# Kernel tuning notes

Measured on AMD Instinct MI355X. Metric: run time of the kernel, lower is better.

Reference implementation:

```python
import jax, jax.numpy as jnp
import numpy as np

N = 4096          # num_nodes
F = 64            # node_features
H = 128           # hidden_dim
NH = 4            # num_heads
HD = H // NH      # per-head dim = 32
L = 3             # num_layers
C = 7             # num_classes
EDGE_P = 0.004    # ~16 avg degree


def setup_inputs() -> dict:
    key = jax.random.key(0)
    ks = jax.random.split(key, 20)
    g = lambda k, shape, fan_in: jax.random.normal(k, shape, jnp.float32) / np.sqrt(fan_in)
    x = jax.random.normal(ks[0], (N, F), jnp.float32)
    adj = (jax.random.uniform(ks[1], (N, N)) < EDGE_P).astype(jnp.float32)
    return {
        "x": x,
        "adj": adj,
        "enc_W": g(ks[2], (F, H), F), "enc_b": jnp.zeros((H,), jnp.float32),
        "gcn_W": g(ks[3], (L, H, H), H), "gcn_b": jnp.zeros((L, H), jnp.float32),
        "attn_W": g(ks[4], (L, NH, H, HD), H), "attn_Wb": jnp.zeros((L, NH, HD), jnp.float32),
        "attn_a": g(ks[5], (L, NH, 2 * HD), 2 * HD), "attn_ab": jnp.zeros((L, NH), jnp.float32),
        "cls_W1": g(ks[6], (H, H // 2), H), "cls_b1": jnp.zeros((H // 2,), jnp.float32),
        "cls_W2": g(ks[7], (H // 2, C), H // 2), "cls_b2": jnp.zeros((C,), jnp.float32),
        "con_W1": g(ks[8], (H, H // 2), H), "con_b1": jnp.zeros((H // 2,), jnp.float32),
        "con_W2": g(ks[9], (H // 2, 1), H // 2), "con_b2": jnp.zeros((1,), jnp.float32),
    }


def _normalize_adj(adj):
    a = adj + jnp.eye(adj.shape[0], dtype=adj.dtype)
    dinv = jnp.sum(a, axis=1) ** -0.5
    return dinv[:, None] * a * dinv[None, :]


def _gcn(h, adj_norm, W, b):
    support = adj_norm @ h                      # [N,H]
    return jax.nn.relu(support @ W + b)         # dropout=0 (eval)


def _attention(h, edge_mask, W, Wb, a, ab):
    # h:[N,H], W:[NH,H,HD], a:[NH,2*HD]; per-pair score = Linear(concat(h_i,h_j))
    hh = jnp.einsum('nf,hfd->hnd', h, W) + Wb[:, None, :]     # [NH,N,HD]
    a_src, a_dst = a[:, :HD], a[:, HD:]
    s_src = jnp.einsum('hnd,hd->hn', hh, a_src)               # [NH,N]
    s_dst = jnp.einsum('hnd,hd->hn', hh, a_dst)               # [NH,N]
    scores = s_src[:, :, None] + s_dst[:, None, :] + ab[:, None, None]
    # original uses literal 0.0 (NOT -inf) for non-edges before softmax
    scores = jnp.where(edge_mask[None, :, :], scores, 0.0)    # [NH,N,N]
    probs = jax.nn.softmax(scores, axis=-1)
    out = jnp.einsum('hij,hjd->hid', probs, hh)               # [NH,N,HD]
    return out.transpose(1, 0, 2).reshape(h.shape[0], NH * HD)


def reference(x, adj, enc_W, enc_b, gcn_W, gcn_b, attn_W, attn_Wb, attn_a, attn_ab,
              cls_W1, cls_b1, cls_W2, cls_b2, con_W1, con_b1, con_W2, con_b2):
    h = jax.nn.relu(x @ enc_W + enc_b)          # node encoder (dropout=0)
    adj_norm = _normalize_adj(adj)
    edge_mask = adj > 0
    for i in range(L):
        h_gcn = _gcn(h, adj_norm, gcn_W[i], gcn_b[i])
        h_attn = _attention(h, edge_mask, attn_W[i], attn_Wb[i], attn_a[i], attn_ab[i])
        h = jax.nn.relu(h_gcn + h_attn)
    node_logits = jax.nn.relu(h @ cls_W1 + cls_b1) @ cls_W2 + cls_b2
    h_mean = jnp.mean(h, axis=0, keepdims=True)
    contagion = jax.nn.relu(h_mean @ con_W1 + con_b1) @ con_W2 + con_b2
    return (node_logits, h, contagion)
```

## Files before the change

kernel.cpp:

```cpp
#include <hip/hip_runtime.h>

typedef unsigned short u16;
typedef unsigned int u32;

#define N 4096
#define F 64
#define H 128
#define NH 4
#define HD 32
#define EMAX 64

__device__ float g_hA[N * H];
__device__ float g_hB[N * H];
__device__ float g_hhA[N * H];
__device__ float g_hhB[N * H];
__device__ u16   g_cols[N * EMAX];
__device__ int   g_deg[N];
__device__ float g_dinv[N];
__device__ float g_ssrcA[N * NH];
__device__ float g_ssrcB[N * NH];
__device__ float g_sdstA[N * NH];
__device__ float g_sdstB[N * NH];
__device__ float g_part[3][32][H];
__device__ float g_hpart[32][H];

__device__ __forceinline__ void agg4(int i0, int tid, const float* __restrict__ h,
                                     const float* __restrict__ hhin,
                                     const float* __restrict__ ssrc_in,
                                     const float* __restrict__ sdst_in,
                                     int l, const float* __restrict__ abv,
                                     int (&jl)[4][EMAX], float (&dv)[4][EMAX],
                                     float (&sdl)[4][EMAX * NH],
                                     float& outa0, float& outa1,
                                     float& sup0, float& sup1) {
  int c = tid & 127, rg = tid >> 7, hc = c >> 5;
  int darr[4];
#pragma unroll
  for (int r = 0; r < 4; ++r) darr[r] = g_deg[i0 + r];
#pragma unroll
  for (int r = 0; r < 4; ++r) {
    const u16* cl = g_cols + (size_t)(i0 + r) * EMAX;
    for (int e = tid; e < darr[r]; e += 256) {
      int j = cl[e];
      jl[r][e] = j;
      dv[r][e] = g_dinv[j];
    }
  }
  __syncthreads();
#pragma unroll
  for (int r = 0; r < 4; ++r)
    for (int idx = tid; idx < darr[r] * NH; idx += 256)
      sdl[r][idx] = sdst_in[jl[r][idx >> 2] * NH + (idx & 3)];
  __syncthreads();

  float sumc = 0.f;
  const float* part = &g_part[l][0][0];
#pragma unroll
  for (int s = 0; s < 32; ++s) sumc += part[s * H + c];
  float ab = abv[hc];

  float oa[2], sp[2];
#pragma unroll
  for (int rr = 0; rr < 2; ++rr) {
    int r = rg * 2 + rr;
    int i = i0 + r, dd = darr[r];
    float ssrc = ssrc_in[i * NH + hc];
    float M = -INFINITY;
    for (int e = 0; e < dd; ++e) M = fmaxf(M, sdl[r][e * NH + hc]);
    float mv = fmaxf(0.f, ssrc + ab + M);
    float em = expf(-mv);
    float base = ssrc + ab - mv;
    float aA = 0.f, aT = 0.f, aG = 0.f, S = 0.f;
    int e = 0;
    for (; e + 2 <= dd; e += 2) {
      int j0 = jl[r][e], j1 = jl[r][e + 1];
      float q0 = hhin[j0 * H + c], q1 = hhin[j1 * H + c];
      float p0 = h[j0 * H + c], p1 = h[j1 * H + c];
      float w0 = expf(base + sdl[r][e * NH + hc]);
      float w1 = expf(base + sdl[r][(e + 1) * NH + hc]);
      aA = fmaf(w0, q0, aA); aA = fmaf(w1, q1, aA);
      aT += q0 + q1;
      aG = fmaf(dv[r][e], p0, aG); aG = fmaf(dv[r][e + 1], p1, aG);
      S += w0 + w1;
    }
    for (; e < dd; ++e) {
      int j = jl[r][e];
      float w = expf(base + sdl[r][e * NH + hc]);
      float q = hhin[j * H + c];
      aA = fmaf(w, q, aA);
      aT += q;
      aG = fmaf(dv[r][e], h[j * H + c], aG);
      S += w;
    }
    float Z = S + em * (float)(N - dd);
    oa[rr] = (aA + em * (sumc - aT)) / Z;
    float di = g_dinv[i];
    sp[rr] = di * (aG + di * h[i * H + c]);
  }
  outa0 = oa[0]; outa1 = oa[1]; sup0 = sp[0]; sup1 = sp[1];
}

__device__ __forceinline__ void proj4(int i0, int tid, const float (&hrowT)[H][4],
                                      const float* __restrict__ aW,
                                      const float* __restrict__ aWb,
                                      const float* __restrict__ aa, int lp,
                                      float* __restrict__ hhout,
                                      float* __restrict__ ssrc_out,
                                      float* __restrict__ sdst_out) {
  int c = tid & 127, rg = tid >> 7, hc = c >> 5, dc = c & 31;
  float b = aWb[hc * HD + dc];
  float p0 = b, p1 = b;
  for (int f = 0; f < H; ++f) {
    float w = aW[(hc * H + f) * HD + dc];
    float2 hv = *reinterpret_cast<const float2*>(&hrowT[f][rg * 2]);
    p0 = fmaf(hv.x, w, p0);
    p1 = fmaf(hv.y, w, p1);
  }
  int r0 = i0 + rg * 2, r1 = r0 + 1;
  hhout[r0 * H + c] = p0;
  hhout[r1 * H + c] = p1;
  const float* ap = aa + hc * 2 * HD;
  float as = ap[dc], ad = ap[HD + dc];
  float ss0 = p0 * as, ss1 = p1 * as, sd0 = p0 * ad, sd1 = p1 * ad;
#pragma unroll
  for (int m = 16; m >= 1; m >>= 1) {
    ss0 += __shfl_xor(ss0, m, 64); ss1 += __shfl_xor(ss1, m, 64);
    sd0 += __shfl_xor(sd0, m, 64); sd1 += __shfl_xor(sd1, m, 64);
  }
  if (dc == 0) {
    ssrc_out[r0 * NH + hc] = ss0; ssrc_out[r1 * NH + hc] = ss1;
    sdst_out[r0 * NH + hc] = sd0; sdst_out[r1 * NH + hc] = sd1;
  }
  atomicAdd(&g_part[lp][r0 & 31][c], p0);
  atomicAdd(&g_part[lp][r1 & 31][c], p1);
}

__global__ void k_prep(const float* __restrict__ adj, const float* __restrict__ x,
                       const float* __restrict__ eW, const float* __restrict__ eb,
                       const float* __restrict__ aW, const float* __restrict__ aWb,
                       const float* __restrict__ aa) {
  __shared__ float xT[F][4];
  __shared__ float hrowT[H][4];
  __shared__ int   cnt4[4];
  int i0 = blockIdx.x * 4, tid = threadIdx.x;
  int c = tid & 127, rg = tid >> 7;

  if (tid < 4) cnt4[tid] = 0;
  __syncthreads();
  {
    int r = tid >> 6, u = tid & 63;
    int row = i0 + r;
    const float4* p = reinterpret_cast<const float4*>(adj + (size_t)row * N) + u;
#pragma unroll
    for (int k = 0; k < 16; ++k) {
      float4 v = p[k * 64];
      int base = (u + k * 64) * 4;
      if (v.x != 0.f) { int q = atomicAdd(&cnt4[r], 1); if (q < EMAX) g_cols[row * EMAX + q] = (u16)(base); }
      if (v.y != 0.f) { int q = atomicAdd(&cnt4[r], 1); if (q < EMAX) g_cols[row * EMAX + q] = (u16)(base + 1); }
      if (v.z != 0.f) { int q = atomicAdd(&cnt4[r], 1); if (q < EMAX) g_cols[row * EMAX + q] = (u16)(base + 2); }
      if (v.w != 0.f) { int q = atomicAdd(&cnt4[r], 1); if (q < EMAX) g_cols[row * EMAX + q] = (u16)(base + 3); }
    }
    xT[tid & 63][tid >> 6] = x[(i0 + (tid >> 6)) * F + (tid & 63)];
  }
  __syncthreads();
  if (tid < 4) {
    int cnt = cnt4[tid];
    g_deg[i0 + tid] = cnt < EMAX ? cnt : EMAX;
    g_dinv[i0 + tid] = 1.0f / sqrtf((float)(cnt + 1));
  }

  float b = eb[c];
  float e0 = b, e1 = b;
  for (int k = 0; k < F; ++k) {
    float w = eW[k * H + c];
    float2 xv = *reinterpret_cast<const float2*>(&xT[k][rg * 2]);
    e0 = fmaf(xv.x, w, e0);
    e1 = fmaf(xv.y, w, e1);
  }
  e0 = fmaxf(e0, 0.f); e1 = fmaxf(e1, 0.f);
  int r0 = i0 + rg * 2, r1 = r0 + 1;
  g_hA[r0 * H + c] = e0; g_hA[r1 * H + c] = e1;
  hrowT[c][rg * 2] = e0; hrowT[c][rg * 2 + 1] = e1;
  __syncthreads();
  proj4(i0, tid, hrowT, aW, aWb, aa, 0, g_hhA, g_ssrcA, g_sdstA);
}

__global__ void k_acp(int pp, int l, const float* __restrict__ gW,
                      const float* __restrict__ gb, const float* __restrict__ aW,
                      const float* __restrict__ aWb, const float* __restrict__ aa,
                      const float* __restrict__ abv) {
  const float* h    = pp ? g_hB : g_hA;
  float*       hout = pp ? g_hA : g_hB;
  const float* hhin = pp ? g_hhB : g_hhA;
  float*       hhout= pp ? g_hhA : g_hhB;
  const float* ssin = pp ? g_ssrcB : g_ssrcA;
  float*       ssout= pp ? g_ssrcA : g_ssrcB;
  const float* sdin = pp ? g_sdstB : g_sdstA;
  float*       sdout= pp ? g_sdstA : g_sdstB;
  __shared__ int   jl[4][EMAX];
  __shared__ float dv[4][EMAX];
  __shared__ float sdl[4][EMAX * NH];
  __shared__ float srowT[H][4];
  __shared__ float hrowT[H][4];
  int i0 = blockIdx.x * 4, tid = threadIdx.x;
  int c = tid & 127, rg = tid >> 7;

  float oa0, oa1, sp0, sp1;
  agg4(i0, tid, h, hhin, ssin, sdin, l, abv, jl, dv, sdl, oa0, oa1, sp0, sp1);
  srowT[c][rg * 2] = sp0; srowT[c][rg * 2 + 1] = sp1;
  __syncthreads();

  float b = gb[c];
  float a0 = b, a1 = b;
  for (int f = 0; f < H; ++f) {
    float w = gW[f * H + c];
    float2 sv = *reinterpret_cast<const float2*>(&srowT[f][rg * 2]);
    a0 = fmaf(sv.x, w, a0);
    a1 = fmaf(sv.y, w, a1);
  }
  float g0 = fmaxf(fmaxf(a0, 0.f) + oa0, 0.f);
  float g1 = fmaxf(fmaxf(a1, 0.f) + oa1, 0.f);
  int r0 = i0 + rg * 2, r1 = r0 + 1;
  hout[r0 * H + c] = g0; hout[r1 * H + c] = g1;
  hrowT[c][rg * 2] = g0; hrowT[c][rg * 2 + 1] = g1;
  __syncthreads();

  proj4(i0, tid, hrowT, aW, aWb, aa, l + 1, hhout, ssout, sdout);
}

__global__ void k_acc(const float* __restrict__ abv, const float* __restrict__ gW,
                      const float* __restrict__ gb,
                      const float* __restrict__ W1, const float* __restrict__ b1,
                      const float* __restrict__ W2, const float* __restrict__ b2,
                      float* __restrict__ out, float* __restrict__ outh) {
  __shared__ int   jl[4][EMAX];
  __shared__ float dv[4][EMAX];
  __shared__ float sdl[4][EMAX * NH];
  __shared__ float srowT[H][4];
  __shared__ float hrowT[H][4];
  __shared__ float tl[4][64];
  int i0 = blockIdx.x * 4, tid = threadIdx.x;
  int c = tid & 127, rg = tid >> 7;

  float oa0, oa1, sp0, sp1;
  agg4(i0, tid, g_hA, g_hhA, g_ssrcA, g_sdstA, 2, abv, jl, dv, sdl, oa0, oa1, sp0, sp1);
  srowT[c][rg * 2] = sp0; srowT[c][rg * 2 + 1] = sp1;
  __syncthreads();

  float b = gb[c];
  float a0 = b, a1 = b;
  for (int f = 0; f < H; ++f) {
    float w = gW[f * H + c];
    float2 sv = *reinterpret_cast<const float2*>(&srowT[f][rg * 2]);
    a0 = fmaf(sv.x, w, a0);
    a1 = fmaf(sv.y, w, a1);
  }
  float g0 = fmaxf(fmaxf(a0, 0.f) + oa0, 0.f);
  float g1 = fmaxf(fmaxf(a1, 0.f) + oa1, 0.f);
  int r0 = i0 + rg * 2, r1 = r0 + 1;
  outh[r0 * H + c] = g0; outh[r1 * H + c] = g1;
  hrowT[c][rg * 2] = g0; hrowT[c][rg * 2 + 1] = g1;
  atomicAdd(&g_hpart[r0 & 31][c], g0);
  atomicAdd(&g_hpart[r1 & 31][c], g1);
  __syncthreads();

  int u = tid & 63, rr4 = tid >> 6;
  float a2 = b1[u];
  for (int f = 0; f < H; ++f) a2 = fmaf(hrowT[f][rr4], W1[f * 64 + u], a2);
  tl[rr4][u] = fmaxf(a2, 0.f);
  __syncthreads();
  if (tid < 28) {
    int r = tid / 7, j = tid - r * 7;
    float p = b2[j];
    for (int v = 0; v < 64; ++v) p = fmaf(tl[r][v], W2[v * 7 + j], p);
    out[(i0 + r) * 7 + j] = p;
  }
}

__global__ void k_contagion(const float* __restrict__ W1, const float* __restrict__ b1,
                            const float* __restrict__ W2, const float* __restrict__ b2,
                            float* __restrict__ out) {
  __shared__ float hm[H];
  __shared__ float tl[64];
  int tid = threadIdx.x;
  {
    float s = 0.f;
#pragma unroll
    for (int sl = 0; sl < 32; ++sl) s += g_hpart[sl][tid];
    hm[tid] = s * (1.0f / 4096.0f);
  }
  __syncthreads();
  if (tid < 64) {
    float acc = b1[tid];
    for (int f = 0; f < H; ++f) acc = fmaf(hm[f], W1[f * 64 + tid], acc);
    tl[tid] = fmaxf(acc, 0.f);
  }
  __syncthreads();
  if (tid == 0) {
    float p = b2[0];
    for (int v = 0; v < 64; ++v) p = fmaf(tl[v], W2[v], p);
    out[0] = p;
  }
  float* pz = &g_part[0][0][0];
  for (int i = tid; i < 3 * 32 * H; i += 128) pz[i] = 0.f;
  float* hz = &g_hpart[0][0];
  for (int i = tid; i < 32 * H; i += 128) hz[i] = 0.f;
}

extern "C" void kernel_launch(void* const* d_in, const int* in_sizes, int n_in,
                              void* d_out, int out_size, void* d_ws, size_t ws_size,
                              hipStream_t stream) {
  const float* x       = (const float*)d_in[0];
  const float* adj     = (const float*)d_in[1];
  const float* enc_W   = (const float*)d_in[2];
  const float* enc_b   = (const float*)d_in[3];
  const float* gcn_W   = (const float*)d_in[4];
  const float* gcn_b   = (const float*)d_in[5];
  const float* attn_W  = (const float*)d_in[6];
  const float* attn_Wb = (const float*)d_in[7];
  const float* attn_a  = (const float*)d_in[8];
  const float* attn_ab = (const float*)d_in[9];
  const float* cls_W1  = (const float*)d_in[10];
  const float* cls_b1  = (const float*)d_in[11];
  const float* cls_W2  = (const float*)d_in[12];
  const float* cls_b2  = (const float*)d_in[13];
  const float* con_W1  = (const float*)d_in[14];
  const float* con_b1  = (const float*)d_in[15];
  const float* con_W2  = (const float*)d_in[16];
  const float* con_b2  = (const float*)d_in[17];
  (void)in_sizes; (void)n_in; (void)d_ws; (void)ws_size; (void)out_size;

  float* out = (float*)d_out;
  float* outh = out + (size_t)N * 7;
  float* outc = out + (size_t)N * 7 + (size_t)N * H;

  k_prep<<<N / 4, 256, 0, stream>>>(adj, x, enc_W, enc_b, attn_W, attn_Wb, attn_a);
  k_acp<<<N / 4, 256, 0, stream>>>(0, 0, gcn_W, gcn_b,
                                   attn_W + (size_t)1 * NH * H * HD,
                                   attn_Wb + (size_t)1 * NH * HD,
                                   attn_a + (size_t)1 * NH * 2 * HD, attn_ab);
  k_acp<<<N / 4, 256, 0, stream>>>(1, 1, gcn_W + (size_t)1 * H * H, gcn_b + H,
                                   attn_W + (size_t)2 * NH * H * HD,
                                   attn_Wb + (size_t)2 * NH * HD,
                                   attn_a + (size_t)2 * NH * 2 * HD, attn_ab + NH);
  k_acc<<<N / 4, 256, 0, stream>>>(attn_ab + 2 * NH, gcn_W + (size_t)2 * H * H,
                                   gcn_b + 2 * H, cls_W1, cls_b1, cls_W2, cls_b2,
                                   out, outh);
  k_contagion<<<1, 128, 0, stream>>>(con_W1, con_b1, con_W2, con_b2, outc);
}
```

Baseline: 232.6 us.

## Process eight rows per block with two columns per thread and float2 loads

Each block now handles 8 nodes instead of 4, and each thread owns two adjacent feature columns, using float2 loads and stores for gathers, weights and outputs. Each weight load now feeds four FMAs instead of two, which cuts weight-read traffic per node and halves the block count. Shared arrays are padded to width 10. The price is more registers per thread and fewer blocks (512) to spread across CUs, which may lower latency hiding in the gather-heavy aggregation.

```diff
diff --git a/kernel.cpp b/kernel.cpp
--- a/kernel.cpp
+++ b/kernel.cpp
@@ -9,6 +9,8 @@
 #define NH 4
 #define HD 32
 #define EMAX 64
+#define BR 8
+#define PAD 10
 
 __device__ float g_hA[N * H];
 __device__ float g_hB[N * H];
@@ -24,23 +26,66 @@
 __device__ float g_part[3][32][H];
 __device__ float g_hpart[32][H];
 
-__device__ __forceinline__ void agg4(int i0, int tid, const float* __restrict__ h,
+__device__ __forceinline__ void proj8(int i0, int tid, const float (&hrowT)[H][PAD],
+                                      const float* __restrict__ aW,
+                                      const float* __restrict__ aWb,
+                                      const float* __restrict__ aa, int lp,
+                                      float* __restrict__ hhout,
+                                      float* __restrict__ ssrc_out,
+                                      float* __restrict__ sdst_out) {
+  int c2 = tid & 63, rg = tid >> 6;
+  int c0 = c2 * 2, hc = c0 >> 5, dc = c0 & 31;
+  float2 bb = *reinterpret_cast<const float2*>(&aWb[hc * HD + dc]);
+  float p00 = bb.x, p01 = bb.y, p10 = bb.x, p11 = bb.y;
+  for (int f = 0; f < H; ++f) {
+    float2 w = *reinterpret_cast<const float2*>(&aW[(hc * H + f) * HD + dc]);
+    float2 hv = *reinterpret_cast<const float2*>(&hrowT[f][rg * 2]);
+    p00 = fmaf(hv.x, w.x, p00); p01 = fmaf(hv.x, w.y, p01);
+    p10 = fmaf(hv.y, w.x, p10); p11 = fmaf(hv.y, w.y, p11);
+  }
+  int r0 = i0 + rg * 2, r1 = r0 + 1;
+  *reinterpret_cast<float2*>(&hhout[r0 * H + c0]) = make_float2(p00, p01);
+  *reinterpret_cast<float2*>(&hhout[r1 * H + c0]) = make_float2(p10, p11);
+  const float* ap = aa + hc * 2 * HD;
+  float2 as = *reinterpret_cast<const float2*>(&ap[dc]);
+  float2 ad = *reinterpret_cast<const float2*>(&ap[HD + dc]);
+  float ss0 = p00 * as.x + p01 * as.y;
+  float ss1 = p10 * as.x + p11 * as.y;
+  float sd0 = p00 * ad.x + p01 * ad.y;
+  float sd1 = p10 * ad.x + p11 * ad.y;
+#pragma unroll
+  for (int m = 8; m >= 1; m >>= 1) {
+    ss0 += __shfl_xor(ss0, m, 64); ss1 += __shfl_xor(ss1, m, 64);
+    sd0 += __shfl_xor(sd0, m, 64); sd1 += __shfl_xor(sd1, m, 64);
+  }
+  if ((c2 & 15) == 0) {
+    ssrc_out[r0 * NH + hc] = ss0; ssrc_out[r1 * NH + hc] = ss1;
+    sdst_out[r0 * NH + hc] = sd0; sdst_out[r1 * NH + hc] = sd1;
+  }
+  atomicAdd(&g_part[lp][r0 & 31][c0], p00);
+  atomicAdd(&g_part[lp][r0 & 31][c0 + 1], p01);
+  atomicAdd(&g_part[lp][r1 & 31][c0], p10);
+  atomicAdd(&g_part[lp][r1 & 31][c0 + 1], p11);
+}
+
+__device__ __forceinline__ void agg8(int i0, int tid, const float* __restrict__ h,
                                      const float* __restrict__ hhin,
                                      const float* __restrict__ ssrc_in,
                                      const float* __restrict__ sdst_in,
                                      int l, const float* __restrict__ abv,
-                                     int (&jl)[4][EMAX], float (&dv)[4][EMAX],
-                                     float (&sdl)[4][EMAX * NH],
-                                     float& outa0, float& outa1,
-                                     float& sup0, float& sup1) {
-  int c = tid & 127, rg = tid >> 7, hc = c >> 5;
-  int darr[4];
-#pragma unroll
-  for (int r = 0; r < 4; ++r) darr[r] = g_deg[i0 + r];
-#pragma unroll
-  for (int r = 0; r < 4; ++r) {
+                                     int (&jl)[BR][EMAX], float (&dv)[BR][EMAX],
+                                     float (&sdl)[BR][EMAX * NH],
+                                     float2& outa0, float2& outa1,
+                                     float2& sup0, float2& sup1) {
+  int c2 = tid & 63, rg = tid >> 6;
+  int c0 = c2 * 2, hc = c0 >> 5;
+  int dloc[BR];
+#pragma unroll
+  for (int r = 0; r < BR; ++r) dloc[r] = g_deg[i0 + r];
+#pragma unroll
+  for (int r = 0; r < BR; ++r) {
     const u16* cl = g_cols + (size_t)(i0 + r) * EMAX;
-    for (int e = tid; e < darr[r]; e += 256) {
+    for (int e = tid; e < dloc[r]; e += 256) {
       int j = cl[e];
       jl[r][e] = j;
       dv[r][e] = g_dinv[j];
@@ -48,141 +93,122 @@
   }
   __syncthreads();
 #pragma unroll
-  for (int r = 0; r < 4; ++r)
-    for (int idx = tid; idx < darr[r] * NH; idx += 256)
+  for (int r = 0; r < BR; ++r)
+    for (int idx = tid; idx < dloc[r] * NH; idx += 256)
       sdl[r][idx] = sdst_in[jl[r][idx >> 2] * NH + (idx & 3)];
   __syncthreads();
 
-  float sumc = 0.f;
+  float sumc0 = 0.f, sumc1 = 0.f;
   const float* part = &g_part[l][0][0];
 #pragma unroll
-  for (int s = 0; s < 32; ++s) sumc += part[s * H + c];
+  for (int s = 0; s < 32; ++s) {
+    sumc0 += part[s * H + c0];
+    sumc1 += part[s * H + c0 + 1];
+  }
   float ab = abv[hc];
 
-  float oa[2], sp[2];
+  float2 oa[2], sp[2];
 #pragma unroll
   for (int rr = 0; rr < 2; ++rr) {
     int r = rg * 2 + rr;
-    int i = i0 + r, dd = darr[r];
+    int i = i0 + r, dd = dloc[r];
     float ssrc = ssrc_in[i * NH + hc];
     float M = -INFINITY;
     for (int e = 0; e < dd; ++e) M = fmaxf(M, sdl[r][e * NH + hc]);
     float mv = fmaxf(0.f, ssrc + ab + M);
     float em = expf(-mv);
     float base = ssrc + ab - mv;
-    float aA = 0.f, aT = 0.f, aG = 0.f, S = 0.f;
+    float aA0 = 0.f, aA1 = 0.f, aT0 = 0.f, aT1 = 0.f, aG0 = 0.f, aG1 = 0.f, S = 0.f;
     int e = 0;
     for (; e + 2 <= dd; e += 2) {
       int j0 = jl[r][e], j1 = jl[r][e + 1];
-      float q0 = hhin[j0 * H + c], q1 = hhin[j1 * H + c];
-      float p0 = h[j0 * H + c], p1 = h[j1 * H + c];
+      float2 q0 = *reinterpret_cast<const float2*>(&hhin[j0 * H + c0]);
+      float2 q1 = *reinterpret_cast<const float2*>(&hhin[j1 * H + c0]);
+      float2 p0 = *reinterpret_cast<const float2*>(&h[j0 * H + c0]);
+      float2 p1 = *reinterpret_cast<const float2*>(&h[j1 * H + c0]);
       float w0 = expf(base + sdl[r][e * NH + hc]);
       float w1 = expf(base + sdl[r][(e + 1) * NH + hc]);
-      aA = fmaf(w0, q0, aA); aA = fmaf(w1, q1, aA);
-      aT += q0 + q1;
-      aG = fmaf(dv[r][e], p0, aG); aG = fmaf(dv[r][e + 1], p1, aG);
+      aA0 = fmaf(w0, q0.x, aA0); aA0 = fmaf(w1, q1.x, aA0);
+      aA1 = fmaf(w0, q0.y, aA1); aA1 = fmaf(w1, q1.y, aA1);
+      aT0 += q0.x + q1.x; aT1 += q0.y + q1.y;
+      aG0 = fmaf(dv[r][e], p0.x, aG0); aG0 = fmaf(dv[r][e + 1], p1.x, aG0);
+      aG1 = fmaf(dv[r][e], p0.y, aG1); aG1 = fmaf(dv[r][e + 1], p1.y, aG1);
       S += w0 + w1;
     }
     for (; e < dd; ++e) {
       int j = jl[r][e];
+      float2 q = *reinterpret_cast<const float2*>(&hhin[j * H + c0]);
+      float2 p = *reinterpret_cast<const float2*>(&h[j * H + c0]);
       float w = expf(base + sdl[r][e * NH + hc]);
-      float q = hhin[j * H + c];
-      aA = fmaf(w, q, aA);
-      aT += q;
-      aG = fmaf(dv[r][e], h[j * H + c], aG);
+      aA0 = fmaf(w, q.x, aA0); aA1 = fmaf(w, q.y, aA1);
+      aT0 += q.x; aT1 += q.y;
+      aG0 = fmaf(dv[r][e], p.x, aG0); aG1 = fmaf(dv[r][e], p.y, aG1);
       S += w;
     }
     float Z = S + em * (float)(N - dd);
-    oa[rr] = (aA + em * (sumc - aT)) / Z;
+    oa[rr] = make_float2((aA0 + em * (sumc0 - aT0)) / Z,
+                         (aA1 + em * (sumc1 - aT1)) / Z);
     float di = g_dinv[i];
-    sp[rr] = di * (aG + di * h[i * H + c]);
+    float2 hvi = *reinterpret_cast<const float2*>(&h[i * H + c0]);
+    sp[rr] = make_float2(di * (aG0 + di * hvi.x), di * (aG1 + di * hvi.y));
   }
   outa0 = oa[0]; outa1 = oa[1]; sup0 = sp[0]; sup1 = sp[1];
-}
-
-__device__ __forceinline__ void proj4(int i0, int tid, const float (&hrowT)[H][4],
-                                      const float* __restrict__ aW,
-                                      const float* __restrict__ aWb,
-                                      const float* __restrict__ aa, int lp,
-                                      float* __restrict__ hhout,
-                                      float* __restrict__ ssrc_out,
-                                      float* __restrict__ sdst_out) {
-  int c = tid & 127, rg = tid >> 7, hc = c >> 5, dc = c & 31;
-  float b = aWb[hc * HD + dc];
-  float p0 = b, p1 = b;
-  for (int f = 0; f < H; ++f) {
-    float w = aW[(hc * H + f) * HD + dc];
-    float2 hv = *reinterpret_cast<const float2*>(&hrowT[f][rg * 2]);
-    p0 = fmaf(hv.x, w, p0);
-    p1 = fmaf(hv.y, w, p1);
-  }
-  int r0 = i0 + rg * 2, r1 = r0 + 1;
-  hhout[r0 * H + c] = p0;
-  hhout[r1 * H + c] = p1;
-  const float* ap = aa + hc * 2 * HD;
-  float as = ap[dc], ad = ap[HD + dc];
-  float ss0 = p0 * as, ss1 = p1 * as, sd0 = p0 * ad, sd1 = p1 * ad;
-#pragma unroll
-  for (int m = 16; m >= 1; m >>= 1) {
-    ss0 += __shfl_xor(ss0, m, 64); ss1 += __shfl_xor(ss1, m, 64);
-    sd0 += __shfl_xor(sd0, m, 64); sd1 += __shfl_xor(sd1, m, 64);
-  }
-  if (dc == 0) {
-    ssrc_out[r0 * NH + hc] = ss0; ssrc_out[r1 * NH + hc] = ss1;
-    sdst_out[r0 * NH + hc] = sd0; sdst_out[r1 * NH + hc] = sd1;
-  }
-  atomicAdd(&g_part[lp][r0 & 31][c], p0);
-  atomicAdd(&g_part[lp][r1 & 31][c], p1);
 }
 
 __global__ void k_prep(const float* __restrict__ adj, const float* __restrict__ x,
                        const float* __restrict__ eW, const float* __restrict__ eb,
                        const float* __restrict__ aW, const float* __restrict__ aWb,
                        const float* __restrict__ aa) {
-  __shared__ float xT[F][4];
-  __shared__ float hrowT[H][4];
-  __shared__ int   cnt4[4];
-  int i0 = blockIdx.x * 4, tid = threadIdx.x;
-  int c = tid & 127, rg = tid >> 7;
-
-  if (tid < 4) cnt4[tid] = 0;
+  __shared__ float xT[F][PAD];
+  __shared__ float hrowT[H][PAD];
+  __shared__ int   cnt8[BR];
+  int i0 = blockIdx.x * BR, tid = threadIdx.x;
+  int c2 = tid & 63, rg = tid >> 6, c0 = c2 * 2;
+
+  if (tid < BR) cnt8[tid] = 0;
   __syncthreads();
   {
-    int r = tid >> 6, u = tid & 63;
+    int r = tid >> 5, u = tid & 31;
     int row = i0 + r;
     const float4* p = reinterpret_cast<const float4*>(adj + (size_t)row * N) + u;
 #pragma unroll
-    for (int k = 0; k < 16; ++k) {
-      float4 v = p[k * 64];
-      int base = (u + k * 64) * 4;
-      if (v.x != 0.f) { int q = atomicAdd(&cnt4[r], 1); if (q < EMAX) g_cols[row * EMAX + q] = (u16)(base); }
-      if (v.y != 0.f) { int q = atomicAdd(&cnt4[r], 1); if (q < EMAX) g_cols[row * EMAX + q] = (u16)(base + 1); }
-      if (v.z != 0.f) { int q = atomicAdd(&cnt4[r], 1); if (q < EMAX) g_cols[row * EMAX + q] = (u16)(base + 2); }
-      if (v.w != 0.f) { int q = atomicAdd(&cnt4[r], 1); if (q < EMAX) g_cols[row * EMAX + q] = (u16)(base + 3); }
+    for (int k = 0; k < 32; ++k) {
+      float4 v = p[k * 32];
+      int base = (u + k * 32) * 4;
+      if (v.x != 0.f) { int q = atomicAdd(&cnt8[r], 1); if (q < EMAX) g_cols[row * EMAX + q] = (u16)(base); }
+      if (v.y != 0.f) { int q = atomicAdd(&cnt8[r], 1); if (q < EMAX) g_cols[row * EMAX + q] = (u16)(base + 1); }
+      if (v.z != 0.f) { int q = atomicAdd(&cnt8[r], 1); if (q < EMAX) g_cols[row * EMAX + q] = (u16)(base + 2); }
+      if (v.w != 0.f) { int q = atomicAdd(&cnt8[r], 1); if (q < EMAX) g_cols[row * EMAX + q] = (u16)(base + 3); }
     }
-    xT[tid & 63][tid >> 6] = x[(i0 + (tid >> 6)) * F + (tid & 63)];
-  }
-  __syncthreads();
-  if (tid < 4) {
-    int cnt = cnt4[tid];
+  }
+  for (int idx = tid; idx < F * BR; idx += 256) {
+    int r = idx & 7, k = idx >> 3;
+    xT[k][r] = x[(i0 + r) * F + k];
+  }
+  __syncthreads();
+  if (tid < BR) {
+    int cnt = cnt8[tid];
     g_deg[i0 + tid] = cnt < EMAX ? cnt : EMAX;
     g_dinv[i0 + tid] = 1.0f / sqrtf((float)(cnt + 1));
   }
 
-  float b = eb[c];
-  float e0 = b, e1 = b;
+  float2 bb = *reinterpret_cast<const float2*>(&eb[c0]);
+  float a00 = bb.x, a01 = bb.y, a10 = bb.x, a11 = bb.y;
   for (int k = 0; k < F; ++k) {
-    float w = eW[k * H + c];
+    float2 w = *reinterpret_cast<const float2*>(&eW[k * H + c0]);
     float2 xv = *reinterpret_cast<const float2*>(&xT[k][rg * 2]);
-    e0 = fmaf(xv.x, w, e0);
-    e1 = fmaf(xv.y, w, e1);
-  }
-  e0 = fmaxf(e0, 0.f); e1 = fmaxf(e1, 0.f);
+    a00 = fmaf(xv.x, w.x, a00); a01 = fmaf(xv.x, w.y, a01);
+    a10 = fmaf(xv.y, w.x, a10); a11 = fmaf(xv.y, w.y, a11);
+  }
+  a00 = fmaxf(a00, 0.f); a01 = fmaxf(a01, 0.f);
+  a10 = fmaxf(a10, 0.f); a11 = fmaxf(a11, 0.f);
   int r0 = i0 + rg * 2, r1 = r0 + 1;
-  g_hA[r0 * H + c] = e0; g_hA[r1 * H + c] = e1;
-  hrowT[c][rg * 2] = e0; hrowT[c][rg * 2 + 1] = e1;
-  __syncthreads();
-  proj4(i0, tid, hrowT, aW, aWb, aa, 0, g_hhA, g_ssrcA, g_sdstA);
+  *reinterpret_cast<float2*>(&g_hA[r0 * H + c0]) = make_float2(a00, a01);
+  *reinterpret_cast<float2*>(&g_hA[r1 * H + c0]) = make_float2(a10, a11);
+  hrowT[c0][rg * 2] = a00; hrowT[c0 + 1][rg * 2] = a01;
+  hrowT[c0][rg * 2 + 1] = a10; hrowT[c0 + 1][rg * 2 + 1] = a11;
+  __syncthreads();
+  proj8(i0, tid, hrowT, aW, aWb, aa, 0, g_hhA, g_ssrcA, g_sdstA);
 }
 
 __global__ void k_acp(int pp, int l, const float* __restrict__ gW,
@@ -197,35 +223,40 @@
   float*       ssout= pp ? g_ssrcA : g_ssrcB;
   const float* sdin = pp ? g_sdstB : g_sdstA;
   float*       sdout= pp ? g_sdstA : g_sdstB;
-  __shared__ int   jl[4][EMAX];
-  __shared__ float dv[4][EMAX];
-  __shared__ float sdl[4][EMAX * NH];
-  __shared__ float srowT[H][4];
-  __shared__ float hrowT[H][4];
-  int i0 = blockIdx.x * 4, tid = threadIdx.x;
-  int c = tid & 127, rg = tid >> 7;
-
-  float oa0, oa1, sp0, sp1;
-  agg4(i0, tid, h, hhin, ssin, sdin, l, abv, jl, dv, sdl, oa0, oa1, sp0, sp1);
-  srowT[c][rg * 2] = sp0; srowT[c][rg * 2 + 1] = sp1;
-  __syncthreads();
-
-  float b = gb[c];
-  float a0 = b, a1 = b;
+  __shared__ int   jl[BR][EMAX];
+  __shared__ float dv[BR][EMAX];
+  __shared__ float sdl[BR][EMAX * NH];
+  __shared__ float srowT[H][PAD];
+  __shared__ float hrowT[H][PAD];
+  int i0 = blockIdx.x * BR, tid = threadIdx.x;
+  int c2 = tid & 63, rg = tid >> 6, c0 = c2 * 2;
+
+  float2 oa0, oa1, sp0, sp1;
+  agg8(i0, tid, h, hhin, ssin, sdin, l, abv, jl, dv, sdl, oa0, oa1, sp0, sp1);
+  srowT[c0][rg * 2] = sp0.x; srowT[c0 + 1][rg * 2] = sp0.y;
+  srowT[c0][rg * 2 + 1] = sp1.x; srowT[c0 + 1][rg * 2 + 1] = sp1.y;
+  __syncthreads();
+
+  float2 bb = *reinterpret_cast<const float2*>(&gb[c0]);
+  float a00 = bb.x, a01 = bb.y, a10 = bb.x, a11 = bb.y;
   for (int f = 0; f < H; ++f) {
-    float w = gW[f * H + c];
+    float2 w = *reinterpret_cast<const float2*>(&gW[f * H + c0]);
     float2 sv = *reinterpret_cast<const float2*>(&srowT[f][rg * 2]);
-    a0 = fmaf(sv.x, w, a0);
-    a1 = fmaf(sv.y, w, a1);
-  }
-  float g0 = fmaxf(fmaxf(a0, 0.f) + oa0, 0.f);
-  float g1 = fmaxf(fmaxf(a1, 0.f) + oa1, 0.f);
+    a00 = fmaf(sv.x, w.x, a00); a01 = fmaf(sv.x, w.y, a01);
+    a10 = fmaf(sv.y, w.x, a10); a11 = fmaf(sv.y, w.y, a11);
+  }
+  float g00 = fmaxf(fmaxf(a00, 0.f) + oa0.x, 0.f);
+  float g01 = fmaxf(fmaxf(a01, 0.f) + oa0.y, 0.f);
+  float g10 = fmaxf(fmaxf(a10, 0.f) + oa1.x, 0.f);
+  float g11 = fmaxf(fmaxf(a11, 0.f) + oa1.y, 0.f);
   int r0 = i0 + rg * 2, r1 = r0 + 1;
-  hout[r0 * H + c] = g0; hout[r1 * H + c] = g1;
-  hrowT[c][rg * 2] = g0; hrowT[c][rg * 2 + 1] = g1;
-  __syncthreads();
-
-  proj4(i0, tid, hrowT, aW, aWb, aa, l + 1, hhout, ssout, sdout);
+  *reinterpret_cast<float2*>(&hout[r0 * H + c0]) = make_float2(g00, g01);
+  *reinterpret_cast<float2*>(&hout[r1 * H + c0]) = make_float2(g10, g11);
+  hrowT[c0][rg * 2] = g00; hrowT[c0 + 1][rg * 2] = g01;
+  hrowT[c0][rg * 2 + 1] = g10; hrowT[c0 + 1][rg * 2 + 1] = g11;
+  __syncthreads();
+
+  proj8(i0, tid, hrowT, aW, aWb, aa, l + 1, hhout, ssout, sdout);
 }
 
 __global__ void k_acc(const float* __restrict__ abv, const float* __restrict__ gW,
@@ -233,43 +264,56 @@
                       const float* __restrict__ W1, const float* __restrict__ b1,
                       const float* __restrict__ W2, const float* __restrict__ b2,
                       float* __restrict__ out, float* __restrict__ outh) {
-  __shared__ int   jl[4][EMAX];
-  __shared__ float dv[4][EMAX];
-  __shared__ float sdl[4][EMAX * NH];
-  __shared__ float srowT[H][4];
-  __shared__ float hrowT[H][4];
-  __shared__ float tl[4][64];
-  int i0 = blockIdx.x * 4, tid = threadIdx.x;
-  int c = tid & 127, rg = tid >> 7;
-
-  float oa0, oa1, sp0, sp1;
-  agg4(i0, tid, g_hA, g_hhA, g_ssrcA, g_sdstA, 2, abv, jl, dv, sdl, oa0, oa1, sp0, sp1);
-  srowT[c][rg * 2] = sp0; srowT[c][rg * 2 + 1] = sp1;
-  __syncthreads();
-
-  float b = gb[c];
-  float a0 = b, a1 = b;
+  __shared__ int   jl[BR][EMAX];
+  __shared__ float dv[BR][EMAX];
+  __shared__ float sdl[BR][EMAX * NH];
+  __shared__ float srowT[H][PAD];
+  __shared__ float hrowT[H][PAD];
+  __shared__ float tl[BR][64];
+  int i0 = blockIdx.x * BR, tid = threadIdx.x;
+  int c2 = tid & 63, rg = tid >> 6, c0 = c2 * 2;
+
+  float2 oa0, oa1, sp0, sp1;
+  agg8(i0, tid, g_hA, g_hhA, g_ssrcA, g_sdstA, 2, abv, jl, dv, sdl, oa0, oa1, sp0, sp1);
+  srowT[c0][rg * 2] = sp0.x; srowT[c0 + 1][rg * 2] = sp0.y;
+  srowT[c0][rg * 2 + 1] = sp1.x; srowT[c0 + 1][rg * 2 + 1] = sp1.y;
+  __syncthreads();
+
+  float2 bb = *reinterpret_cast<const float2*>(&gb[c0]);
+  float a00 = bb.x, a01 = bb.y, a10 = bb.x, a11 = bb.y;
   for (int f = 0; f < H; ++f) {
-    float w = gW[f * H + c];
+    float2 w = *reinterpret_cast<const float2*>(&gW[f * H + c0]);
     float2 sv = *reinterpret_cast<const float2*>(&srowT[f][rg * 2]);
-    a0 = fmaf(sv.x, w, a0);
-    a1 = fmaf(sv.y, w, a1);
-  }
-  float g0 = fmaxf(fmaxf(a0, 0.f) + oa0, 0.f);
-  float g1 = fmaxf(fmaxf(a1, 0.f) + oa1, 0.f);
+    a00 = fmaf(sv.x, w.x, a00); a01 = fmaf(sv.x, w.y, a01);
+    a10 = fmaf(sv.y, w.x, a10); a11 = fmaf(sv.y, w.y, a11);
+  }
+  float g00 = fmaxf(fmaxf(a00, 0.f) + oa0.x, 0.f);
+  float g01 = fmaxf(fmaxf(a01, 0.f) + oa0.y, 0.f);
+  float g10 = fmaxf(fmaxf(a10, 0.f) + oa1.x, 0.f);
+  float g11 = fmaxf(fmaxf(a11, 0.f) + oa1.y, 0.f);
   int r0 = i0 + rg * 2, r1 = r0 + 1;
-  outh[r0 * H + c] = g0; outh[r1 * H + c] = g1;
-  hrowT[c][rg * 2] = g0; hrowT[c][rg * 2 + 1] = g1;
-  atomicAdd(&g_hpart[r0 & 31][c], g0);
-  atomicAdd(&g_hpart[r1 & 31][c], g1);
-  __syncthreads();
-
-  int u = tid & 63, rr4 = tid >> 6;
-  float a2 = b1[u];
-  for (int f = 0; f < H; ++f) a2 = fmaf(hrowT[f][rr4], W1[f * 64 + u], a2);
-  tl[rr4][u] = fmaxf(a2, 0.f);
-  __syncthreads();
-  if (tid < 28) {
+  *reinterpret_cast<float2*>(&outh[r0 * H + c0]) = make_float2(g00, g01);
+  *reinterpret_cast<float2*>(&outh[r1 * H + c0]) = make_float2(g10, g11);
+  hrowT[c0][rg * 2] = g00; hrowT[c0 + 1][rg * 2] = g01;
+  hrowT[c0][rg * 2 + 1] = g10; hrowT[c0 + 1][rg * 2 + 1] = g11;
+  atomicAdd(&g_hpart[r0 & 31][c0], g00);
+  atomicAdd(&g_hpart[r0 & 31][c0 + 1], g01);
+  atomicAdd(&g_hpart[r1 & 31][c0], g10);
+  atomicAdd(&g_hpart[r1 & 31][c0 + 1], g11);
+  __syncthreads();
+
+  int u = tid & 63, wv = tid >> 6;
+  float aA = b1[u], aB = b1[u];
+  for (int f = 0; f < H; ++f) {
+    float w = W1[f * 64 + u];
+    float2 hv = *reinterpret_cast<const float2*>(&hrowT[f][wv * 2]);
+    aA = fmaf(hv.x, w, aA);
+    aB = fmaf(hv.y, w, aB);
+  }
+  tl[wv * 2][u] = fmaxf(aA, 0.f);
+  tl[wv * 2 + 1][u] = fmaxf(aB, 0.f);
+  __syncthreads();
+  if (tid < BR * 7) {
     int r = tid / 7, j = tid - r * 7;
     float p = b2[j];
     for (int v = 0; v < 64; ++v) p = fmaf(tl[r][v], W2[v * 7 + j], p);
@@ -334,17 +378,17 @@
   float* outh = out + (size_t)N * 7;
   float* outc = out + (size_t)N * 7 + (size_t)N * H;
 
-  k_prep<<<N / 4, 256, 0, stream>>>(adj, x, enc_W, enc_b, attn_W, attn_Wb, attn_a);
-  k_acp<<<N / 4, 256, 0, stream>>>(0, 0, gcn_W, gcn_b,
-                                   attn_W + (size_t)1 * NH * H * HD,
-                                   attn_Wb + (size_t)1 * NH * HD,
-                                   attn_a + (size_t)1 * NH * 2 * HD, attn_ab);
-  k_acp<<<N / 4, 256, 0, stream>>>(1, 1, gcn_W + (size_t)1 * H * H, gcn_b + H,
-                                   attn_W + (size_t)2 * NH * H * HD,
-                                   attn_Wb + (size_t)2 * NH * HD,
-                                   attn_a + (size_t)2 * NH * 2 * HD, attn_ab + NH);
-  k_acc<<<N / 4, 256, 0, stream>>>(attn_ab + 2 * NH, gcn_W + (size_t)2 * H * H,
-                                   gcn_b + 2 * H, cls_W1, cls_b1, cls_W2, cls_b2,
-                                   out, outh);
+  k_prep<<<N / BR, 256, 0, stream>>>(adj, x, enc_W, enc_b, attn_W, attn_Wb, attn_a);
+  k_acp<<<N / BR, 256, 0, stream>>>(0, 0, gcn_W, gcn_b,
+                                    attn_W + (size_t)1 * NH * H * HD,
+                                    attn_Wb + (size_t)1 * NH * HD,
+                                    attn_a + (size_t)1 * NH * 2 * HD, attn_ab);
+  k_acp<<<N / BR, 256, 0, stream>>>(1, 1, gcn_W + (size_t)1 * H * H, gcn_b + H,
+                                    attn_W + (size_t)2 * NH * H * HD,
+                                    attn_Wb + (size_t)2 * NH * HD,
+                                    attn_a + (size_t)2 * NH * 2 * HD, attn_ab + NH);
+  k_acc<<<N / BR, 256, 0, stream>>>(attn_ab + 2 * NH, gcn_W + (size_t)2 * H * H,
+                                    gcn_b + 2 * H, cls_W1, cls_b1, cls_W2, cls_b2,
+                                    out, outh);
   k_contagion<<<1, 128, 0, stream>>>(con_W1, con_b1, con_W2, con_b2, outc);
 }
```

New measurement: 312.4 us. 34.3% more time.
